# Optimization experiments

Measured on AMD Instinct MI355X. Metric: run time of the kernel, lower is better.

Reference implementation:

```python
import jax, jax.numpy as jnp
import numpy as np

NUM_HEADS = 16
ROPE_THETA = 10000.0


def _rope_tables(T, head_dim, dtype=jnp.float32):
    # Standard rotate-half RoPE tables: [T, head_dim]
    half = head_dim // 2
    inv_freq = 1.0 / (ROPE_THETA ** (jnp.arange(0, half, dtype=jnp.float32) / half))
    ang = jnp.arange(T, dtype=jnp.float32)[:, None] * inv_freq[None, :]  # [T, half]
    cos = jnp.concatenate([jnp.cos(ang), jnp.cos(ang)], axis=-1).astype(dtype)
    sin = jnp.concatenate([jnp.sin(ang), jnp.sin(ang)], axis=-1).astype(dtype)
    return cos, sin


def _apply_rope(x, cos, sin):
    # x: [B, T, H, D]; cos/sin: [T, D]
    D = x.shape[-1]
    x1, x2 = x[..., : D // 2], x[..., D // 2 :]
    rotated = jnp.concatenate([-x2, x1], axis=-1)
    return x * cos[None, :, None, :] + rotated * sin[None, :, None, :]


def setup_inputs() -> dict:
    key = jax.random.key(0)
    k1, k2, k3 = jax.random.split(key, 3)
    B, T, C = 4, 2048, 2048
    x = jax.random.normal(k1, (B, T, C), dtype=jnp.float32)
    w_attn = jax.random.normal(k2, (C, 3 * C), dtype=jnp.float32) * 0.02
    w_proj = jax.random.normal(k3, (C, C), dtype=jnp.float32) * 0.02
    return {"x": x, "w_attn": w_attn, "w_proj": w_proj}


def reference(x, w_attn, w_proj):
    B, T, C = x.shape
    H = NUM_HEADS
    D = C // H

    qkv = x @ w_attn                         # [B, T, 3C]
    q, k, v = jnp.split(qkv, 3, axis=-1)
    q = q.reshape(B, T, H, D)
    k = k.reshape(B, T, H, D)
    v = v.reshape(B, T, H, D)

    cos, sin = _rope_tables(T, D, x.dtype)
    q = _apply_rope(q, cos, sin)
    k = _apply_rope(k, cos, sin)

    # causal SDPA, heads-first layout [B, H, T, D]
    scale = 1.0 / jnp.sqrt(jnp.asarray(D, dtype=x.dtype))
    scores = jnp.einsum("bqhd,bkhd->bhqk", q, k) * scale  # [B, H, T, T]
    causal = jnp.tril(jnp.ones((T, T), dtype=bool))
    scores = jnp.where(causal[None, None], scores, jnp.finfo(scores.dtype).min)
    attn = jax.nn.softmax(scores, axis=-1)
    y = jnp.einsum("bhqk,bkhd->bqhd", attn, v).reshape(B, T, C)
    return y @ w_proj
```

## Files before the change

### kernel.cpp

```cpp
#include <hip/hip_runtime.h>

typedef __bf16 bf16;
typedef __bf16 bf16x8 __attribute__((ext_vector_type(8)));
typedef __bf16 bf16x4 __attribute__((ext_vector_type(4)));
typedef __bf16 bf16x2 __attribute__((ext_vector_type(2)));
typedef float floatx4 __attribute__((ext_vector_type(4)));
typedef float floatx16 __attribute__((ext_vector_type(16)));

#define NB 4
#define NT 2048
#define NC 2048
#define NH 16
#define ND 128
#define QKS 4096

__device__ __forceinline__ void load_lds16(const void* gptr, void* ldsptr) {
  __builtin_amdgcn_global_load_lds(
      (const __attribute__((address_space(1))) unsigned int*)gptr,
      (__attribute__((address_space(3))) unsigned int*)ldsptr, 16, 0, 0);
}

__device__ __forceinline__ unsigned pack2(float a, float b) {
  bf16x2 v;
  v[0] = (bf16)a; v[1] = (bf16)b;
  return __builtin_bit_cast(unsigned, v);
}

__global__ __launch_bounds__(256) void cast_f32_bf16(const float* __restrict__ in,
                                                     bf16* __restrict__ out) {
  const int i = blockIdx.x * 256 + threadIdx.x;
  const float4 v = ((const float4*)in)[i];
  bf16x4 o;
  o[0] = (bf16)v.x; o[1] = (bf16)v.y; o[2] = (bf16)v.z; o[3] = (bf16)v.w;
  ((bf16x4*)out)[i] = o;
}

__global__ __launch_bounds__(256) void transpose_cast(const float* __restrict__ in,
                                                      bf16* __restrict__ out,
                                                      int R, int Cc) {
  __shared__ float tile[128][65];
  const int r0 = blockIdx.y * 128, c0 = blockIdx.x * 64;
  const int rr = threadIdx.x >> 6, cc = threadIdx.x & 63;
#pragma unroll
  for (int i = 0; i < 32; ++i)
    tile[rr + i * 4][cc] = in[(size_t)(r0 + rr + i * 4) * Cc + c0 + cc];
  __syncthreads();
  const int rv = threadIdx.x & 63, halfr = (threadIdx.x >> 6) & 1, crh = threadIdx.x >> 7;
#pragma unroll
  for (int i = 0; i < 32; ++i) {
    const int cr = crh * 32 + i;
    out[(size_t)(c0 + cr) * R + r0 + halfr * 64 + rv] = (bf16)tile[halfr * 64 + rv][cr];
  }
}

template <int EPI, typename OutT>
__global__ __launch_bounds__(256) void gemm_bt(const bf16* __restrict__ A,
                                               const bf16* __restrict__ Bt,
                                               OutT* __restrict__ C,
                                               bf16* __restrict__ qk,
                                               bf16* __restrict__ vt,
                                               int M, int N, int K, int NTX) {
  __shared__ bf16 smem[128 * 132];
  __shared__ float invf_s[64];
  bf16* As = smem;
  bf16* Bs = smem + 128 * 64;
  const int tid = threadIdx.x;
  const int w = tid >> 6, l = tid & 63, quad = l >> 4, l16 = l & 15;
  const int wm = (w >> 1) * 64, wn = (w & 1) * 64;

  const int per = 8 * NTX;
  const int band = blockIdx.x / per, rem = blockIdx.x - band * per;
  const int by = band * 8 + (rem & 7), bx = rem >> 3;
  const int m0 = by * 128, n0 = bx * 128;

  if (EPI == 1 && tid < 64)
    invf_s[tid] = exp2f(-(float)tid * 0.20762050593046014f);

  const floatx4 fzero = {0.f, 0.f, 0.f, 0.f};
  floatx4 acc[4][4];
#pragma unroll
  for (int i = 0; i < 4; ++i)
#pragma unroll
    for (int j = 0; j < 4; ++j) acc[i][j] = fzero;

  for (int k0 = 0; k0 < K; k0 += 64) {
#pragma unroll
    for (int i = 0; i < 4; ++i) {
      const int fb = (w * 4 + i) * 64;
      const int f = fb + l;
      const int r = f >> 3, cs = f & 7, c = cs ^ (r & 7);
      load_lds16(A + (size_t)(m0 + r) * K + k0 + c * 8, As + fb * 8);
      load_lds16(Bt + (size_t)(n0 + r) * K + k0 + c * 8, Bs + fb * 8);
    }
    __syncthreads();
#pragma unroll
    for (int kk = 0; kk < 2; ++kk) {
      bf16x8 af[4], bfr[4];
#pragma unroll
      for (int mi = 0; mi < 4; ++mi) {
        const int row = wm + mi * 16 + l16;
        af[mi] = *(const bf16x8*)(As + row * 64 + ((kk * 4 + quad) ^ (row & 7)) * 8);
      }
#pragma unroll
      for (int ni = 0; ni < 4; ++ni) {
        const int row = wn + ni * 16 + l16;
        bfr[ni] = *(const bf16x8*)(Bs + row * 64 + ((kk * 4 + quad) ^ (row & 7)) * 8);
      }
#pragma unroll
      for (int mi = 0; mi < 4; ++mi)
#pragma unroll
        for (int ni = 0; ni < 4; ++ni)
          acc[mi][ni] = __builtin_amdgcn_mfma_f32_16x16x32_bf16(af[mi], bfr[ni],
                                                                acc[mi][ni], 0, 0, 0);
    }
    __syncthreads();
  }

  if constexpr (EPI == 0) {
#pragma unroll
    for (int mi = 0; mi < 4; ++mi)
#pragma unroll
      for (int ni = 0; ni < 4; ++ni) {
        const int row = m0 + wm + mi * 16 + quad * 4;
        const int col = n0 + wn + ni * 16 + l16;
#pragma unroll
        for (int r = 0; r < 4; ++r)
          C[(size_t)(row + r) * N + col] = (OutT)acc[mi][ni][r];
      }
  } else {
    bf16* Tl = smem;
#pragma unroll
    for (int mi = 0; mi < 4; ++mi)
#pragma unroll
      for (int ni = 0; ni < 4; ++ni) {
        const int rloc = wm + mi * 16 + quad * 4;
        const int cloc = wn + ni * 16 + l16;
#pragma unroll
        for (int r = 0; r < 4; ++r)
          Tl[(rloc + r) * 130 + cloc] = (bf16)acc[mi][ni][r];
      }
    __syncthreads();

    const int nt = n0 >> 7;
    if (nt < 32) {
      const int r = tid >> 1, hd = tid & 1;
      const int t = (m0 & (NT - 1)) + r;
      const float tt = (float)t;
      bf16* dst = qk + (size_t)(m0 + r) * QKS + n0;
#pragma unroll
      for (int j8 = 0; j8 < 2; ++j8) {
        const int d0 = hd * 32 + j8 * 16;
        bf16x8 lo[2], hi[2];
#pragma unroll
        for (int half8 = 0; half8 < 2; ++half8) {
#pragma unroll
          for (int jj = 0; jj < 8; ++jj) {
            const int d = d0 + half8 * 8 + jj;
            const float x1 = (float)Tl[r * 130 + d];
            const float x2 = (float)Tl[r * 130 + d + 64];
            float s, c;
            __sincosf(tt * invf_s[d], &s, &c);
            lo[half8][jj] = (bf16)(x1 * c - x2 * s);
            hi[half8][jj] = (bf16)(x2 * c + x1 * s);
          }
          *(bf16x8*)(dst + d0 + half8 * 8) = lo[half8];
          *(bf16x8*)(dst + d0 + half8 * 8 + 64) = hi[half8];
        }
      }
    } else {
      const int h = nt - 32;
      const int b = m0 >> 11;
      const int t0 = m0 & (NT - 1);
      const int vbase = (b * NH + h) * ND;
#pragma unroll
      for (int ii = 0; ii < 8; ++ii) {
        const int dd = (tid >> 4) + ii * 16;
        const int ch = tid & 15;
        bf16x8 o;
#pragma unroll
        for (int j = 0; j < 8; ++j) o[j] = Tl[(ch * 8 + j) * 130 + dd];
        *(bf16x8*)(vt + (size_t)(vbase + dd) * NT + t0 + ch * 8) = o;
      }
    }
  }
}

__global__ __launch_bounds__(256) void attn_kernel(const bf16* __restrict__ qk,
                                                   const bf16* __restrict__ vt,
                                                   bf16* __restrict__ y) {
  __shared__ bf16 Ks[2][64 * 128];
  __shared__ bf16 Vs[2][128 * 64];

  const int pair = blockIdx.x, h = blockIdx.y, b = blockIdx.z;
  const int tid = threadIdx.x;
  const int w = tid >> 6, l = tid & 63, half = l >> 5, l32 = l & 31;
  const float SCL = 0.08838834764831845f * 1.4426950408889634f;

#pragma unroll 1
  for (int pi = 0; pi < 2; ++pi) {
    const int qt = pi ? (15 - pair) : pair;
    const int q0 = qt * 128;
    const int ntiles = qt * 2 + 2;
    const int qg = q0 + w * 32 + l32;

    bf16x8 aq[8];
#pragma unroll
    for (int ks = 0; ks < 8; ++ks)
      aq[ks] = *(const bf16x8*)(qk + (size_t)(b * NT + qg) * QKS + h * ND + ks * 16 + half * 8);

    floatx16 acc[4];
#pragma unroll
    for (int ni = 0; ni < 4; ++ni)
#pragma unroll
      for (int r = 0; r < 16; ++r) acc[ni][r] = 0.f;
    float mold = -3.0e38f, lsum = 0.f;

    {
#pragma unroll
      for (int i = 0; i < 4; ++i) {
        const int fb = i * 256 + w * 64, f = fb + l;
        { const int r = f >> 4, cs = f & 15, c = cs ^ (r & 15);
          load_lds16(qk + (size_t)(b * NT + r) * QKS + NC + h * ND + c * 8, &Ks[0][fb * 8]); }
        { const int r = f >> 3, cs = f & 7, c = cs ^ (r & 7);
          load_lds16(vt + ((size_t)((b * NH + h) * ND + r)) * NT + c * 8, &Vs[0][fb * 8]); }
      }
    }

#pragma unroll 1
    for (int it = 0; it < ntiles; ++it) {
      const int kv0 = it * 64;
      const int buf = it & 1;
      __syncthreads();

      if (it + 1 < ntiles) {
        const int kvn = kv0 + 64, nb = buf ^ 1;
#pragma unroll
        for (int i = 0; i < 4; ++i) {
          const int fb = i * 256 + w * 64, f = fb + l;
          { const int r = f >> 4, cs = f & 15, c = cs ^ (r & 15);
            load_lds16(qk + (size_t)(b * NT + kvn + r) * QKS + NC + h * ND + c * 8, &Ks[nb][fb * 8]); }
          { const int r = f >> 3, cs = f & 7, c = cs ^ (r & 7);
            load_lds16(vt + ((size_t)((b * NH + h) * ND + r)) * NT + kvn + c * 8, &Vs[nb][fb * 8]); }
        }
      }

      if (kv0 <= q0 + w * 32 + 31) {
        floatx16 st[2];
#pragma unroll
        for (int ki = 0; ki < 2; ++ki)
#pragma unroll
          for (int r = 0; r < 16; ++r) st[ki][r] = 0.f;
#pragma unroll
        for (int ks = 0; ks < 8; ++ks) {
          const int slot = (ks * 2 + half) ^ (l32 & 15);
#pragma unroll
          for (int ki = 0; ki < 2; ++ki) {
            const bf16x8 ak = *(const bf16x8*)(&Ks[buf][(ki * 32 + l32) * 128 + slot * 8]);
            st[ki] = __builtin_amdgcn_mfma_f32_32x32x16_bf16(ak, aq[ks], st[ki], 0, 0, 0);
          }
        }

        float mx = -3.0e38f;
        if (kv0 + 63 > q0 + w * 32) {
#pragma unroll
          for (int ki = 0; ki < 2; ++ki)
#pragma unroll
            for (int r = 0; r < 16; ++r) {
              const int kg = kv0 + ki * 32 + (r & 3) + 8 * (r >> 2) + 4 * half;
              float s = st[ki][r] * SCL;
              s = (kg > qg) ? -3.0e38f : s;
              st[ki][r] = s;
              mx = fmaxf(mx, s);
            }
        } else {
#pragma unroll
          for (int ki = 0; ki < 2; ++ki)
#pragma unroll
            for (int r = 0; r < 16; ++r) {
              const float s = st[ki][r] * SCL;
              st[ki][r] = s;
              mx = fmaxf(mx, s);
            }
        }
        mx = fmaxf(mx, __shfl_xor(mx, 32));

        const float mnew = fmaxf(mold, mx);
        const float al = exp2f(mold - mnew);
        float rs = 0.f;
#pragma unroll
        for (int ki = 0; ki < 2; ++ki)
#pragma unroll
          for (int r = 0; r < 16; ++r) {
            const float p = exp2f(st[ki][r] - mnew);
            st[ki][r] = p;
            rs += p;
          }
        rs += __shfl_xor(rs, 32);
        lsum = lsum * al + rs;
        mold = mnew;
#pragma unroll
        for (int ni = 0; ni < 4; ++ni)
#pragma unroll
          for (int r = 0; r < 16; ++r) acc[ni][r] *= al;

        unsigned pk[2][8];
#pragma unroll
        for (int ki = 0; ki < 2; ++ki)
#pragma unroll
          for (int d = 0; d < 8; ++d)
            pk[ki][d] = pack2(st[ki][2 * d], st[ki][2 * d + 1]);
        bf16x8 bp[4];
#pragma unroll
        for (int s = 0; s < 4; ++s) {
          const int ki = s >> 1, o = (s & 1) * 4;
          const unsigned a0 = pk[ki][o], a1 = pk[ki][o + 1], a2 = pk[ki][o + 2], a3 = pk[ki][o + 3];
          const unsigned s0 = (unsigned)__shfl_xor((int)a0, 32);
          const unsigned s1 = (unsigned)__shfl_xor((int)a1, 32);
          const unsigned s2 = (unsigned)__shfl_xor((int)a2, 32);
          const unsigned s3 = (unsigned)__shfl_xor((int)a3, 32);
          uint4 dw;
          dw.x = half ? s2 : a0;
          dw.y = half ? s3 : a1;
          dw.z = half ? a2 : s0;
          dw.w = half ? a3 : s1;
          bp[s] = __builtin_bit_cast(bf16x8, dw);
        }

#pragma unroll
        for (int ni = 0; ni < 4; ++ni) {
          const int rv = ni * 32 + l32;
#pragma unroll
          for (int s = 0; s < 4; ++s) {
            const int slot = (s * 2 + half) ^ (l32 & 7);
            const bf16x8 av = *(const bf16x8*)(&Vs[buf][rv * 64 + slot * 8]);
            acc[ni] = __builtin_amdgcn_mfma_f32_32x32x16_bf16(av, bp[s], acc[ni], 0, 0, 0);
          }
        }
      }
    }

    const float inv = 1.f / lsum;
    const size_t orow = (size_t)(b * NT + qg) * NC + h * ND;
#pragma unroll
    for (int ni = 0; ni < 4; ++ni)
#pragma unroll
      for (int rg = 0; rg < 4; ++rg) {
        bf16x4 o;
#pragma unroll
        for (int j = 0; j < 4; ++j) o[j] = (bf16)(acc[ni][rg * 4 + j] * inv);
        *(bf16x4*)(y + orow + ni * 32 + rg * 8 + half * 4) = o;
      }
    __syncthreads();
  }
}

extern "C" void kernel_launch(void* const* d_in, const int* in_sizes, int n_in,
                              void* d_out, int out_size, void* d_ws, size_t ws_size,
                              hipStream_t stream) {
  const float* x      = (const float*)d_in[0];
  const float* w_attn = (const float*)d_in[1];
  const float* w_proj = (const float*)d_in[2];
  float* out = (float*)d_out;
  char* ws = (char*)d_ws;

  bf16* qk  = (bf16*)(ws);
  bf16* vt  = (bf16*)(ws + 67108864);
  bf16* xb  = (bf16*)(ws + 100663296);
  bf16* wab = (bf16*)(ws + 134217728);
  bf16* y   = wab;
  bf16* wpb = (bf16*)(ws + 167772160);

  cast_f32_bf16<<<dim3(16384), dim3(256), 0, stream>>>(x, xb);
  transpose_cast<<<dim3(96, 16), dim3(256), 0, stream>>>(w_attn, wab, 2048, 6144);
  transpose_cast<<<dim3(32, 16), dim3(256), 0, stream>>>(w_proj, wpb, 2048, 2048);
  gemm_bt<1, float><<<dim3(3072), dim3(256), 0, stream>>>(xb, wab, (float*)nullptr, qk, vt,
                                                          8192, 6144, 2048, 48);
  attn_kernel<<<dim3(8, 16, 4), dim3(256), 0, stream>>>(qk, vt, y);
  gemm_bt<0, float><<<dim3(1024), dim3(256), 0, stream>>>(y, wpb, out, nullptr, nullptr,
                                                          8192, 2048, 2048, 16);
}
```

Measured before the change: 663.2 us.

## Rewrite GEMM with 256x256 tiles, double-buffered LDS and XCD-aware block remap

```diff
diff --git a/kernel.cpp b/kernel.cpp
--- a/kernel.cpp
+++ b/kernel.cpp
@@ -53,134 +53,206 @@
   }
 }
 
+__device__ __forceinline__ void stage_half(bf16* lds, const bf16* __restrict__ g,
+                                           int row0, int k0, int h, int K,
+                                           int w, int l) {
+#pragma unroll
+  for (int i = 0; i < 2; ++i) {
+    const int fb = h * 1024 + w * 128 + i * 64;
+    const int f = fb + l;
+    const int r = f >> 3, cs = f & 7, c = cs ^ (r & 7);
+    load_lds16(g + (size_t)(row0 + r) * K + k0 + c * 8, lds + fb * 8);
+  }
+}
+
 template <int EPI, typename OutT>
-__global__ __launch_bounds__(256) void gemm_bt(const bf16* __restrict__ A,
-                                               const bf16* __restrict__ Bt,
-                                               OutT* __restrict__ C,
-                                               bf16* __restrict__ qk,
-                                               bf16* __restrict__ vt,
-                                               int M, int N, int K, int NTX) {
-  __shared__ bf16 smem[128 * 132];
+__global__ __launch_bounds__(512, 2) void gemm_bt(const bf16* __restrict__ A,
+                                                  const bf16* __restrict__ Bt,
+                                                  OutT* __restrict__ C,
+                                                  bf16* __restrict__ qk,
+                                                  bf16* __restrict__ vt,
+                                                  int M, int N, int K, int NTX) {
+  __shared__ bf16 smem[65536];
   __shared__ float invf_s[64];
-  bf16* As = smem;
-  bf16* Bs = smem + 128 * 64;
   const int tid = threadIdx.x;
   const int w = tid >> 6, l = tid & 63, quad = l >> 4, l16 = l & 15;
-  const int wm = (w >> 1) * 64, wn = (w & 1) * 64;
-
+  const int wm = w >> 2, wn = w & 3;
+
+  const int cpx = gridDim.x >> 3;
+  const int orig = blockIdx.x;
+  const int wgid = (orig & 7) * cpx + (orig >> 3);
   const int per = 8 * NTX;
-  const int band = blockIdx.x / per, rem = blockIdx.x - band * per;
+  const int band = wgid / per, rem = wgid - band * per;
   const int by = band * 8 + (rem & 7), bx = rem >> 3;
-  const int m0 = by * 128, n0 = bx * 128;
+  const int m0 = by * 256, n0 = bx * 256;
 
   if (EPI == 1 && tid < 64)
     invf_s[tid] = exp2f(-(float)tid * 0.20762050593046014f);
 
+  const int KT = K >> 6;
+
   const floatx4 fzero = {0.f, 0.f, 0.f, 0.f};
-  floatx4 acc[4][4];
-#pragma unroll
-  for (int i = 0; i < 4; ++i)
+  floatx4 acc[8][4];
+#pragma unroll
+  for (int i = 0; i < 8; ++i)
 #pragma unroll
     for (int j = 0; j < 4; ++j) acc[i][j] = fzero;
 
-  for (int k0 = 0; k0 < K; k0 += 64) {
-#pragma unroll
-    for (int i = 0; i < 4; ++i) {
-      const int fb = (w * 4 + i) * 64;
-      const int f = fb + l;
-      const int r = f >> 3, cs = f & 7, c = cs ^ (r & 7);
-      load_lds16(A + (size_t)(m0 + r) * K + k0 + c * 8, As + fb * 8);
-      load_lds16(Bt + (size_t)(n0 + r) * K + k0 + c * 8, Bs + fb * 8);
-    }
-    __syncthreads();
-#pragma unroll
-    for (int kk = 0; kk < 2; ++kk) {
-      bf16x8 af[4], bfr[4];
-#pragma unroll
-      for (int mi = 0; mi < 4; ++mi) {
-        const int row = wm + mi * 16 + l16;
-        af[mi] = *(const bf16x8*)(As + row * 64 + ((kk * 4 + quad) ^ (row & 7)) * 8);
-      }
+  {
+    bf16* As0 = smem;           bf16* Bs0 = smem + 16384;
+    bf16* As1 = smem + 32768;
+    stage_half(As0, A, m0, 0, 0, K, w, l);
+    stage_half(As0, A, m0, 0, 1, K, w, l);
+    stage_half(Bs0, Bt, n0, 0, 0, K, w, l);
+    stage_half(Bs0, Bt, n0, 0, 1, K, w, l);
+    if (KT > 1) {
+      stage_half(As1, A, m0, 64, 0, K, w, l);
+      stage_half(As1, A, m0, 64, 1, K, w, l);
+      asm volatile("s_waitcnt vmcnt(4)" ::: "memory");
+    } else {
+      asm volatile("s_waitcnt vmcnt(0)" ::: "memory");
+    }
+    __builtin_amdgcn_sched_barrier(0);
+    __builtin_amdgcn_s_barrier();
+    __builtin_amdgcn_sched_barrier(0);
+  }
+
+#pragma unroll 1
+  for (int t = 0; t < KT; ++t) {
+    const int cur = t & 1;
+    bf16* As_c = smem + cur * 32768;
+    bf16* Bs_c = As_c + 16384;
+    bf16* Bs_n = smem + (cur ^ 1) * 32768 + 16384;
+
+    bf16x8 bfr[2][4];
+#pragma unroll
+    for (int p = 0; p < 4; ++p) {
+      bf16x8 af[2][2];
+#pragma unroll
+      for (int mr = 0; mr < 2; ++mr)
+#pragma unroll
+        for (int ks = 0; ks < 2; ++ks) {
+          const int row = wm * 128 + (p * 2 + mr) * 16 + l16;
+          const int slot = (ks * 4 + quad) ^ (row & 7);
+          af[mr][ks] = *(const bf16x8*)(As_c + row * 64 + slot * 8);
+        }
+      if (p == 0) {
+#pragma unroll
+        for (int ks = 0; ks < 2; ++ks)
+#pragma unroll
+          for (int ni = 0; ni < 4; ++ni) {
+            const int row = wn * 64 + ni * 16 + l16;
+            const int slot = (ks * 4 + quad) ^ (row & 7);
+            bfr[ks][ni] = *(const bf16x8*)(Bs_c + row * 64 + slot * 8);
+          }
+      }
+      if (p < 2 && t + 1 < KT)
+        stage_half(Bs_n, Bt, n0, (t + 1) * 64, p, K, w, l);
+
+      __builtin_amdgcn_s_barrier();
+      asm volatile("s_waitcnt lgkmcnt(0)" ::: "memory");
+      __builtin_amdgcn_sched_barrier(0);
+      __builtin_amdgcn_s_setprio(1);
+#pragma unroll
+      for (int mr = 0; mr < 2; ++mr)
+#pragma unroll
+        for (int ks = 0; ks < 2; ++ks)
+#pragma unroll
+          for (int ni = 0; ni < 4; ++ni)
+            acc[p * 2 + mr][ni] = __builtin_amdgcn_mfma_f32_16x16x32_bf16(
+                af[mr][ks], bfr[ks][ni], acc[p * 2 + mr][ni], 0, 0, 0);
+      __builtin_amdgcn_s_setprio(0);
+      __builtin_amdgcn_s_barrier();
+    }
+
+    if (t + 1 < KT) {
+      if (t + 2 < KT) {
+        stage_half(As_c, A, m0, (t + 2) * 64, 0, K, w, l);
+        stage_half(As_c, A, m0, (t + 2) * 64, 1, K, w, l);
+        asm volatile("s_waitcnt vmcnt(4)" ::: "memory");
+      } else {
+        asm volatile("s_waitcnt vmcnt(0)" ::: "memory");
+      }
+      __builtin_amdgcn_sched_barrier(0);
+      __builtin_amdgcn_s_barrier();
+      __builtin_amdgcn_sched_barrier(0);
+    }
+  }
+
+  if constexpr (EPI == 0) {
+#pragma unroll
+    for (int mi = 0; mi < 8; ++mi)
 #pragma unroll
       for (int ni = 0; ni < 4; ++ni) {
-        const int row = wn + ni * 16 + l16;
-        bfr[ni] = *(const bf16x8*)(Bs + row * 64 + ((kk * 4 + quad) ^ (row & 7)) * 8);
-      }
-#pragma unroll
-      for (int mi = 0; mi < 4; ++mi)
-#pragma unroll
-        for (int ni = 0; ni < 4; ++ni)
-          acc[mi][ni] = __builtin_amdgcn_mfma_f32_16x16x32_bf16(af[mi], bfr[ni],
-                                                                acc[mi][ni], 0, 0, 0);
-    }
-    __syncthreads();
-  }
-
-  if constexpr (EPI == 0) {
-#pragma unroll
-    for (int mi = 0; mi < 4; ++mi)
-#pragma unroll
-      for (int ni = 0; ni < 4; ++ni) {
-        const int row = m0 + wm + mi * 16 + quad * 4;
-        const int col = n0 + wn + ni * 16 + l16;
+        const int row = m0 + wm * 128 + mi * 16 + quad * 4;
+        const int col = n0 + wn * 64 + ni * 16 + l16;
 #pragma unroll
         for (int r = 0; r < 4; ++r)
           C[(size_t)(row + r) * N + col] = (OutT)acc[mi][ni][r];
       }
   } else {
     bf16* Tl = smem;
-#pragma unroll
-    for (int mi = 0; mi < 4; ++mi)
-#pragma unroll
-      for (int ni = 0; ni < 4; ++ni) {
-        const int rloc = wm + mi * 16 + quad * 4;
-        const int cloc = wn + ni * 16 + l16;
-#pragma unroll
-        for (int r = 0; r < 4; ++r)
-          Tl[(rloc + r) * 130 + cloc] = (bf16)acc[mi][ni][r];
-      }
-    __syncthreads();
-
-    const int nt = n0 >> 7;
-    if (nt < 32) {
-      const int r = tid >> 1, hd = tid & 1;
-      const int t = (m0 & (NT - 1)) + r;
-      const float tt = (float)t;
-      bf16* dst = qk + (size_t)(m0 + r) * QKS + n0;
-#pragma unroll
-      for (int j8 = 0; j8 < 2; ++j8) {
-        const int d0 = hd * 32 + j8 * 16;
-        bf16x8 lo[2], hi[2];
-#pragma unroll
-        for (int half8 = 0; half8 < 2; ++half8) {
-#pragma unroll
-          for (int jj = 0; jj < 8; ++jj) {
-            const int d = d0 + half8 * 8 + jj;
-            const float x1 = (float)Tl[r * 130 + d];
-            const float x2 = (float)Tl[r * 130 + d + 64];
-            float s, c;
-            __sincosf(tt * invf_s[d], &s, &c);
-            lo[half8][jj] = (bf16)(x1 * c - x2 * s);
-            hi[half8][jj] = (bf16)(x2 * c + x1 * s);
-          }
-          *(bf16x8*)(dst + d0 + half8 * 8) = lo[half8];
-          *(bf16x8*)(dst + d0 + half8 * 8 + 64) = hi[half8];
-        }
-      }
-    } else {
-      const int h = nt - 32;
-      const int b = m0 >> 11;
-      const int t0 = m0 & (NT - 1);
-      const int vbase = (b * NH + h) * ND;
-#pragma unroll
-      for (int ii = 0; ii < 8; ++ii) {
-        const int dd = (tid >> 4) + ii * 16;
-        const int ch = tid & 15;
-        bf16x8 o;
-#pragma unroll
-        for (int j = 0; j < 8; ++j) o[j] = Tl[(ch * 8 + j) * 130 + dd];
-        *(bf16x8*)(vt + (size_t)(vbase + dd) * NT + t0 + ch * 8) = o;
-      }
+#pragma unroll 1
+    for (int q = 0; q < 2; ++q) {
+      if ((wn >> 1) == q) {
+        bf16* Tg = Tl + wm * (128 * 130);
+#pragma unroll
+        for (int mi = 0; mi < 8; ++mi)
+#pragma unroll
+          for (int ni = 0; ni < 4; ++ni) {
+            const int rl = mi * 16 + quad * 4;
+            const int cl = (wn & 1) * 64 + ni * 16 + l16;
+#pragma unroll
+            for (int r = 0; r < 4; ++r)
+              Tg[(rl + r) * 130 + cl] = (bf16)acc[mi][ni][r];
+          }
+      }
+      __syncthreads();
+
+      const int g = tid >> 8, t8 = tid & 255;
+      const int m0q = m0 + g * 128, n0q = n0 + q * 128;
+      bf16* Tq = Tl + g * (128 * 130);
+      const int nt = n0q >> 7;
+      if (nt < 32) {
+        const int r = t8 >> 1, hd = t8 & 1;
+        const float tt = (float)((m0q & (NT - 1)) + r);
+        bf16* dst = qk + (size_t)(m0q + r) * QKS + n0q;
+#pragma unroll
+        for (int j8 = 0; j8 < 2; ++j8) {
+          const int d0 = hd * 32 + j8 * 16;
+          bf16x8 lo[2], hi[2];
+#pragma unroll
+          for (int half8 = 0; half8 < 2; ++half8) {
+#pragma unroll
+            for (int jj = 0; jj < 8; ++jj) {
+              const int d = d0 + half8 * 8 + jj;
+              const float x1 = (float)Tq[r * 130 + d];
+              const float x2 = (float)Tq[r * 130 + d + 64];
+              float s, c;
+              __sincosf(tt * invf_s[d], &s, &c);
+              lo[half8][jj] = (bf16)(x1 * c - x2 * s);
+              hi[half8][jj] = (bf16)(x2 * c + x1 * s);
+            }
+            *(bf16x8*)(dst + d0 + half8 * 8) = lo[half8];
+            *(bf16x8*)(dst + d0 + half8 * 8 + 64) = hi[half8];
+          }
+        }
+      } else {
+        const int h = nt - 32;
+        const int b = m0q >> 11;
+        const int t0 = m0q & (NT - 1);
+        const int vbase = (b * NH + h) * ND;
+#pragma unroll
+        for (int ii = 0; ii < 8; ++ii) {
+          const int dd = (t8 >> 4) + ii * 16;
+          const int ch = t8 & 15;
+          bf16x8 o;
+#pragma unroll
+          for (int j = 0; j < 8; ++j) o[j] = Tq[(ch * 8 + j) * 130 + dd];
+          *(bf16x8*)(vt + (size_t)(vbase + dd) * NT + t0 + ch * 8) = o;
+        }
+      }
+      __syncthreads();
     }
   }
 }
@@ -373,9 +445,9 @@
   cast_f32_bf16<<<dim3(16384), dim3(256), 0, stream>>>(x, xb);
   transpose_cast<<<dim3(96, 16), dim3(256), 0, stream>>>(w_attn, wab, 2048, 6144);
   transpose_cast<<<dim3(32, 16), dim3(256), 0, stream>>>(w_proj, wpb, 2048, 2048);
-  gemm_bt<1, float><<<dim3(3072), dim3(256), 0, stream>>>(xb, wab, (float*)nullptr, qk, vt,
-                                                          8192, 6144, 2048, 48);
+  gemm_bt<1, float><<<dim3(768), dim3(512), 0, stream>>>(xb, wab, (float*)nullptr, qk, vt,
+                                                         8192, 6144, 2048, 24);
   attn_kernel<<<dim3(8, 16, 4), dim3(256), 0, stream>>>(qk, vt, y);
-  gemm_bt<0, float><<<dim3(1024), dim3(256), 0, stream>>>(y, wpb, out, nullptr, nullptr,
-                                                          8192, 2048, 2048, 16);
-}
+  gemm_bt<0, float><<<dim3(256), dim3(512), 0, stream>>>(y, wpb, out, nullptr, nullptr,
+                                                         8192, 2048, 2048, 8);
+}
```

After: 652.4 us. No clear change (-1.6%).
